# Kernel optimization log

Measured on AMD Instinct MI355X. Metric: run time of the kernel, lower is better.

Reference implementation:

```python
import jax, jax.numpy as jnp
import numpy as np

IN_DIM, OUT_DIM, NUM, K = 64, 16, 5, 3
BATCH = 65536


def extend_grid(grid, k):
    # grid: (in_dim, num+1) uniform; append k points on each side with step h
    h = (grid[:, -1:] - grid[:, :1]) / (grid.shape[1] - 1)
    left = grid[:, :1] - h * jnp.arange(k, 0, -1, dtype=grid.dtype)
    right = grid[:, -1:] + h * jnp.arange(1, k + 1, dtype=grid.dtype)
    return jnp.concatenate([left, grid, right], axis=1)  # (in_dim, num+2k+1)


def b_batch(x, grid, k):
    # Cox-de Boor recursion. x: (B, in_dim), grid: (in_dim, G+2k+1)
    xe = x[:, :, None]          # (B, in, 1)
    g = grid[None, :, :]        # (1, in, G+2k+1)
    B = ((xe >= g[:, :, :-1]) & (xe < g[:, :, 1:])).astype(x.dtype)
    for p in range(1, k + 1):
        B = ((xe - g[:, :, :-(p + 1)]) / (g[:, :, p:-1] - g[:, :, :-(p + 1)]) * B[:, :, :-1]
             + (g[:, :, p + 1:] - xe) / (g[:, :, p + 1:] - g[:, :, 1:-p]) * B[:, :, 1:])
        B = jnp.nan_to_num(B)
    return B  # (B, in, G+k)


def setup_inputs() -> dict:
    key = jax.random.key(0)
    k1, k2, k3 = jax.random.split(key, 3)
    x = jax.random.normal(k1, (BATCH, IN_DIM), dtype=jnp.float32)
    base_grid = jnp.broadcast_to(jnp.linspace(-1.0, 1.0, NUM + 1, dtype=jnp.float32), (IN_DIM, NUM + 1))
    grid = extend_grid(base_grid, K)                       # (in, num+2k+1)
    coef = jax.random.normal(k2, (IN_DIM, OUT_DIM, NUM + K), dtype=jnp.float32) * 0.1
    scale_sp = jnp.ones((IN_DIM, OUT_DIM), dtype=jnp.float32) / np.sqrt(IN_DIM).astype(np.float32)
    scale_base = (jax.random.uniform(k3, (IN_DIM, OUT_DIM), dtype=jnp.float32) * 2.0 - 1.0) / np.sqrt(IN_DIM).astype(np.float32)
    return {"x": x, "grid": grid, "coef": coef, "scale_base": scale_base, "scale_sp": scale_sp}


def reference(x, grid, coef, scale_base, scale_sp):
    bs = x.shape[0]
    preacts = jnp.broadcast_to(x[:, None, :], (bs, OUT_DIM, IN_DIM))
    B = b_batch(x, grid, K)                                # (bs, in, G+k)
    y = jnp.einsum('bik,iok->bio', B, coef)                # coef2curve: (bs, in, out)
    postspline = jnp.transpose(y, (0, 2, 1))               # (bs, out, in)
    base = jax.nn.silu(x)                                  # SiLU base function (include_bias=True)
    y = scale_base[None, :, :] * base[:, :, None] + scale_sp[None, :, :] * y
    postacts = jnp.transpose(y, (0, 2, 1))                 # (bs, out, in)
    out = jnp.sum(y, axis=1)                               # (bs, out)
    return (out, preacts, postacts, postspline)
```

## Files before the change

### kernel.cpp

```cpp
#include <hip/hip_runtime.h>

#define IN_DIM 64
#define OUT_DIM 16
#define NGRID 12
#define NB 8
#define TST 68
#define ROWS 8

typedef _Float16 half2_t __attribute__((ext_vector_type(2)));
typedef float    fx4     __attribute__((ext_vector_type(4)));

__device__ __forceinline__ half2_t pkrtz(float a, float b) {
    return __builtin_bit_cast(half2_t, __builtin_amdgcn_cvt_pkrtz(a, b));
}

__device__ __forceinline__ float dpp_add16(float v) {
    int x = __builtin_bit_cast(int, v);
    v += __builtin_bit_cast(float, __builtin_amdgcn_update_dpp(0, x, 0x118, 0xf, 0xf, true));
    x = __builtin_bit_cast(int, v);
    v += __builtin_bit_cast(float, __builtin_amdgcn_update_dpp(0, x, 0x114, 0xf, 0xf, true));
    x = __builtin_bit_cast(int, v);
    v += __builtin_bit_cast(float, __builtin_amdgcn_update_dpp(0, x, 0x112, 0xf, 0xf, true));
    x = __builtin_bit_cast(int, v);
    v += __builtin_bit_cast(float, __builtin_amdgcn_update_dpp(0, x, 0x111, 0xf, 0xf, true));
    return v;
}

__global__ __launch_bounds__(256, 3) void kan_fwd_kernel(
    const float* __restrict__ x,
    const float* __restrict__ grid,
    const float* __restrict__ coef,
    const float* __restrict__ sbase,
    const float* __restrict__ ssp,
    float* __restrict__ out,
    float* __restrict__ preacts,
    float* __restrict__ postacts,
    float* __restrict__ postspline,
    int batch)
{
    __shared__ float sT[4][OUT_DIM * TST];

    const int tid  = threadIdx.x;
    const int lane = tid & 63;
    const int wave = tid >> 6;
    const int i = lane;

    const long b0 = ((long)blockIdx.x * 4 + wave) * ROWS;
    if (b0 >= batch) return;

    const float g0 = grid[i * NGRID + 0];
    const float g1 = grid[i * NGRID + 1];
    const float invh = 1.0f / (g1 - g0);

    half2_t c[OUT_DIM][4];
    {
        const fx4* c4 = reinterpret_cast<const fx4*>(coef + (size_t)i * OUT_DIM * NB);
        #pragma unroll
        for (int o = 0; o < OUT_DIM; ++o) {
            fx4 a = c4[o * 2], bq = c4[o * 2 + 1];
            c[o][0] = pkrtz(a.x,  a.y);
            c[o][1] = pkrtz(a.z,  a.w);
            c[o][2] = pkrtz(bq.x, bq.y);
            c[o][3] = pkrtz(bq.z, bq.w);
        }
    }

    const int ci = (lane & 15) * 4;
    const int ro = lane >> 4;
    float sbt[4][4], spt[4][4];
    #pragma unroll
    for (int sl = 0; sl < 4; ++sl) {
        const int o = sl * 4 + ro;
        #pragma unroll
        for (int k = 0; k < 4; ++k) {
            sbt[sl][k] = sbase[(ci + k) * OUT_DIM + o];
            spt[sl][k] = ssp  [(ci + k) * OUT_DIM + o];
        }
    }

    float* sTw = sT[wave];
    float xi_cur = x[b0 * IN_DIM + i];

    #pragma unroll 1
    for (int r = 0; r < ROWS; ++r) {
        const long b = b0 + r;
        if (b >= batch) break;
        float xi_next = 0.0f;
        if (r + 1 < ROWS && b + 1 < batch) xi_next = x[(b + 1) * IN_DIM + i];
        const float xi = xi_cur;

        const float t = (xi - g0) * invh;
        float d[NGRID];
        #pragma unroll
        for (int j = 0; j < NGRID; ++j) d[j] = t - (float)j;

        float Bv[11];
        #pragma unroll
        for (int j = 0; j < 11; ++j)
            Bv[j] = (d[j] >= 0.0f && d[j + 1] < 0.0f) ? 1.0f : 0.0f;

        #pragma unroll
        for (int j = 0; j < 10; ++j)
            Bv[j] = d[j] * Bv[j] - d[j + 2] * Bv[j + 1];
        #pragma unroll
        for (int j = 0; j < 9; ++j)
            Bv[j] = (d[j] * Bv[j] - d[j + 3] * Bv[j + 1]) * 0.5f;
        #pragma unroll
        for (int j = 0; j < 8; ++j)
            Bv[j] = (d[j] * Bv[j] - d[j + 4] * Bv[j + 1]) * (1.0f / 3.0f);

        half2_t bh[4];
        #pragma unroll
        for (int q = 0; q < 4; ++q)
            bh[q] = pkrtz(Bv[2 * q], Bv[2 * q + 1]);

        #pragma unroll
        for (int o = 0; o < OUT_DIM; ++o) {
            float y = __builtin_amdgcn_fdot2(c[o][0], bh[0],
                      __builtin_amdgcn_fdot2(c[o][1], bh[1],
                      __builtin_amdgcn_fdot2(c[o][2], bh[2],
                      __builtin_amdgcn_fdot2(c[o][3], bh[3], 0.0f, false),
                      false), false), false);
            sTw[o * TST + i] = y;
        }

        const float base = xi / (1.0f + __expf(-xi));
        fx4 xq, bq;
        xq.x = __shfl(xi, ci + 0, 64);  bq.x = __shfl(base, ci + 0, 64);
        xq.y = __shfl(xi, ci + 1, 64);  bq.y = __shfl(base, ci + 1, 64);
        xq.z = __shfl(xi, ci + 2, 64);  bq.z = __shfl(base, ci + 2, 64);
        xq.w = __shfl(xi, ci + 3, 64);  bq.w = __shfl(base, ci + 3, 64);

        const size_t rowoff = (size_t)b * (OUT_DIM * IN_DIM);
        float ps0, ps1, ps2, ps3;

        #pragma unroll
        for (int sl = 0; sl < 4; ++sl) {
            const int row = sl * 4 + ro;
            fx4 yv = *reinterpret_cast<const fx4*>(&sTw[row * TST + ci]);
            fx4 y2;
            y2.x = __builtin_fmaf(sbt[sl][0], bq.x, spt[sl][0] * yv.x);
            y2.y = __builtin_fmaf(sbt[sl][1], bq.y, spt[sl][1] * yv.y);
            y2.z = __builtin_fmaf(sbt[sl][2], bq.z, spt[sl][2] * yv.z);
            y2.w = __builtin_fmaf(sbt[sl][3], bq.w, spt[sl][3] * yv.w);

            const size_t goff = rowoff + (size_t)sl * 256 + 4 * lane;
            __builtin_nontemporal_store(yv, reinterpret_cast<fx4*>(&postspline[goff]));
            __builtin_nontemporal_store(y2, reinterpret_cast<fx4*>(&postacts[goff]));
            __builtin_nontemporal_store(xq, reinterpret_cast<fx4*>(&preacts[goff]));

            const float ps = (y2.x + y2.y) + (y2.z + y2.w);
            if (sl == 0) ps0 = ps; else if (sl == 1) ps1 = ps;
            else if (sl == 2) ps2 = ps; else ps3 = ps;
        }

        ps0 = dpp_add16(ps0);
        ps1 = dpp_add16(ps1);
        ps2 = dpp_add16(ps2);
        ps3 = dpp_add16(ps3);
        if ((lane & 15) == 15) {
            float* ob = out + (size_t)b * OUT_DIM;
            ob[0  + ro] = ps0;
            ob[4  + ro] = ps1;
            ob[8  + ro] = ps2;
            ob[12 + ro] = ps3;
        }

        xi_cur = xi_next;
    }
}

extern "C" void kernel_launch(void* const* d_in, const int* in_sizes, int n_in,
                              void* d_out, int out_size, void* d_ws, size_t ws_size,
                              hipStream_t stream) {
    const float* x     = (const float*)d_in[0];
    const float* grid  = (const float*)d_in[1];
    const float* coef  = (const float*)d_in[2];
    const float* sbase = (const float*)d_in[3];
    const float* ssp   = (const float*)d_in[4];

    const int batch = in_sizes[0] / IN_DIM;

    float* out = (float*)d_out;
    float* preacts    = out + (size_t)batch * OUT_DIM;
    float* postacts   = preacts  + (size_t)batch * OUT_DIM * IN_DIM;
    float* postspline = postacts + (size_t)batch * OUT_DIM * IN_DIM;

    const int rows_per_block = 4 * ROWS;
    const int nblocks = (batch + rows_per_block - 1) / rows_per_block;
    kan_fwd_kernel<<<nblocks, 256, 0, stream>>>(
        x, grid, coef, sbase, ssp, out, preacts, postacts, postspline, batch);
}
```

Measured before the change: 160.6 us.

## Offload preacts broadcast stores to dedicated copy blocks interleaved with compute blocks

Every third block now only copies x into the broadcast preacts output using vector nontemporal stores. The remaining blocks compute splines and write postspline, postacts and out without the preacts stores or the x shuffles. This is meant to cut per-row store and shuffle work in the compute waves and balance pure memory work against compute work. The grid size is hardcoded to 3072, which ties the kernel to a batch of 65536.

```diff
diff --git a/kernel.cpp b/kernel.cpp
--- a/kernel.cpp
+++ b/kernel.cpp
@@ -40,12 +40,28 @@
 {
     __shared__ float sT[4][OUT_DIM * TST];
 
-    const int tid  = threadIdx.x;
+    const int bid = blockIdx.x;
+    const int tid = threadIdx.x;
+
+    if (bid % 3 == 2) {
+        const int fb = bid / 3;
+        const fx4* __restrict__ xv = reinterpret_cast<const fx4*>(x);
+        const size_t base = (size_t)fb * 16384;
+        #pragma unroll 4
+        for (int s = 0; s < 64; ++s) {
+            const size_t q = base + (size_t)s * 256 + tid;
+            const fx4 v = xv[(q >> 8) * 16 + (q & 15)];
+            __builtin_nontemporal_store(v, reinterpret_cast<fx4*>(&preacts[4 * q]));
+        }
+        return;
+    }
+
+    const int mb = (bid / 3) * 2 + (bid % 3);
     const int lane = tid & 63;
     const int wave = tid >> 6;
     const int i = lane;
 
-    const long b0 = ((long)blockIdx.x * 4 + wave) * ROWS;
+    const long b0 = ((long)mb * 4 + wave) * ROWS;
     if (b0 >= batch) return;
 
     const float g0 = grid[i * NGRID + 0];
@@ -125,11 +141,11 @@
         }
 
         const float base = xi / (1.0f + __expf(-xi));
-        fx4 xq, bq;
-        xq.x = __shfl(xi, ci + 0, 64);  bq.x = __shfl(base, ci + 0, 64);
-        xq.y = __shfl(xi, ci + 1, 64);  bq.y = __shfl(base, ci + 1, 64);
-        xq.z = __shfl(xi, ci + 2, 64);  bq.z = __shfl(base, ci + 2, 64);
-        xq.w = __shfl(xi, ci + 3, 64);  bq.w = __shfl(base, ci + 3, 64);
+        fx4 bq;
+        bq.x = __shfl(base, ci + 0, 64);
+        bq.y = __shfl(base, ci + 1, 64);
+        bq.z = __shfl(base, ci + 2, 64);
+        bq.w = __shfl(base, ci + 3, 64);
 
         const size_t rowoff = (size_t)b * (OUT_DIM * IN_DIM);
         float ps0, ps1, ps2, ps3;
@@ -147,7 +163,6 @@
             const size_t goff = rowoff + (size_t)sl * 256 + 4 * lane;
             __builtin_nontemporal_store(yv, reinterpret_cast<fx4*>(&postspline[goff]));
             __builtin_nontemporal_store(y2, reinterpret_cast<fx4*>(&postacts[goff]));
-            __builtin_nontemporal_store(xq, reinterpret_cast<fx4*>(&preacts[goff]));
 
             const float ps = (y2.x + y2.y) + (y2.z + y2.w);
             if (sl == 0) ps0 = ps; else if (sl == 1) ps1 = ps;
@@ -186,8 +201,7 @@
     float* postacts   = preacts  + (size_t)batch * OUT_DIM * IN_DIM;
     float* postspline = postacts + (size_t)batch * OUT_DIM * IN_DIM;
 
-    const int rows_per_block = 4 * ROWS;
-    const int nblocks = (batch + rows_per_block - 1) / rows_per_block;
+    const int nblocks = 3072;
     kan_fwd_kernel<<<nblocks, 256, 0, stream>>>(
         x, grid, coef, sbase, ssp, out, preacts, postacts, postspline, batch);
 }
```

Result: slower. 168.3 us (+4.8%).
